# Performance work log

Measured on AMD Instinct MI355X. Metric: run time of the kernel, lower is better.

Reference implementation:

```python
import jax, jax.numpy as jnp
import numpy as np

B, S, D, H = 2, 2048, 1024, 16
HD = D // H  # head dim 64

def setup_inputs() -> dict:
    key = jax.random.key(0)
    k1, k2, k3 = jax.random.split(key, 3)
    x = jax.random.normal(k1, (B, S, D), dtype=jnp.float32)
    w_attn = jax.random.normal(k2, (D, 3 * D), dtype=jnp.float32) * (1.0 / np.sqrt(D))
    w_proj = jax.random.normal(k3, (D, D), dtype=jnp.float32) * (1.0 / np.sqrt(D))
    return {"x": x, "w_attn": w_attn, "w_proj": w_proj}

def reference(x, w_attn, w_proj):
    b, s, d = x.shape
    qkv = x @ w_attn                      # [b, s, 3d]
    q, k, v = jnp.split(qkv, 3, axis=-1)
    def heads(t):
        return t.reshape(b, s, H, HD).transpose(0, 2, 1, 3)  # [b, h, s, hd]
    q, k, v = heads(q), heads(k), heads(v)
    scale = 1.0 / np.sqrt(HD)
    att = jnp.einsum('bhqd,bhkd->bhqk', q, k) * scale        # [b, h, s, s]
    causal = jnp.tril(jnp.ones((s, s), dtype=bool))
    att = jnp.where(causal[None, None], att, -jnp.inf)
    att = jax.nn.softmax(att, axis=-1)
    y = jnp.einsum('bhqk,bhkd->bhqd', att, v)                # [b, h, s, hd]
    y = y.transpose(0, 2, 1, 3).reshape(b, s, d)
    return y @ w_proj
```

## Files before the change

kernel.cpp:

```cpp
#include <hip/hip_runtime.h>

#define B_  2
#define S_  2048
#define D_  1024
#define H_  16
#define HD_ 64
#define TD_ 3072

typedef __bf16 bf16x8 __attribute__((ext_vector_type(8)));
typedef float  f32x4  __attribute__((ext_vector_type(4)));
typedef float  f32x16 __attribute__((ext_vector_type(16)));

#define AS1 __attribute__((address_space(1)))
#define AS3 __attribute__((address_space(3)))

#define MASKVAL (-60000.0f)
#define MINITVAL (-30000.0f)

__device__ __forceinline__ unsigned short f2bf(float f) {
  return __builtin_bit_cast(unsigned short, (__bf16)f);
}

__device__ __forceinline__ unsigned int pkbf(float lo, float hi) {
  unsigned int r;
  asm("v_cvt_pk_bf16_f32 %0, %1, %2" : "=v"(r) : "v"(lo), "v"(hi));
  return r;
}

__device__ __forceinline__ void plswap(unsigned int& a, unsigned int& b) {
  asm volatile("v_permlane32_swap_b32 %0, %1" : "+v"(a), "+v"(b));
}

__device__ __forceinline__ float exp2a(float x) {
  return __builtin_amdgcn_exp2f(x);
}

__device__ __forceinline__ float xmax32(float x) {
  return fmaxf(x, __shfl_xor(x, 32, 64));
}
__device__ __forceinline__ float xadd32(float x) {
  return x + __shfl_xor(x, 32, 64);
}

__device__ __forceinline__ void gload16(const void* g, void* l) {
  __builtin_amdgcn_global_load_lds((const AS1 void*)g, (AS3 void*)l, 16, 0, 0);
}

__global__ __launch_bounds__(256) void k_convert_x(const float* __restrict__ x,
                                                   unsigned short* __restrict__ xb) {
  const int i = (blockIdx.x * 256 + threadIdx.x) * 4;
  float4 v = *(const float4*)(x + i);
  ushort4 o;
  o.x = f2bf(v.x); o.y = f2bf(v.y); o.z = f2bf(v.z); o.w = f2bf(v.w);
  *(ushort4*)(xb + i) = o;
}

__global__ __launch_bounds__(256) void k_prep_w(const float* __restrict__ wa,
                                                const float* __restrict__ wp,
                                                unsigned short* __restrict__ waT,
                                                unsigned short* __restrict__ wpT) {
  __shared__ __align__(16) unsigned short tile[64][72];
  const int t = threadIdx.x;
  const int bx = blockIdx.x;
  const float* w;
  unsigned short* wt;
  int C, c0;
  if (bx < 48) { w = wa; wt = waT; C = TD_; c0 = bx * 64; }
  else         { w = wp; wt = wpT; C = D_;  c0 = (bx - 48) * 64; }
  const int R = D_;
  const int r0 = blockIdx.y * 64;
  const int rr = t >> 2, cc = (t & 3) * 16;
  const float* src = w + (size_t)(r0 + rr) * C + c0 + cc;
#pragma unroll
  for (int j = 0; j < 16; j += 4) {
    float4 v = *(const float4*)(src + j);
    tile[rr][cc + j + 0] = f2bf(v.x);
    tile[rr][cc + j + 1] = f2bf(v.y);
    tile[rr][cc + j + 2] = f2bf(v.z);
    tile[rr][cc + j + 3] = f2bf(v.w);
  }
  __syncthreads();
  unsigned short* dst = wt + (size_t)(c0 + rr) * R + r0 + cc;
#pragma unroll
  for (int j = 0; j < 16; j += 2) {
    unsigned int pk = (unsigned int)tile[cc + j][rr] |
                      ((unsigned int)tile[cc + j + 1][rr] << 16);
    *(unsigned int*)(dst + j) = pk;
  }
}

__global__ __launch_bounds__(256) void k_gemm_qkv(const unsigned short* __restrict__ A,
                                                  const unsigned short* __restrict__ Bt,
                                                  unsigned short* __restrict__ qb,
                                                  unsigned short* __restrict__ kp,
                                                  unsigned short* __restrict__ vp) {
  __shared__ __align__(16) unsigned short ldsA[128 * 64];
  __shared__ __align__(16) unsigned short ldsB[128 * 64];
  const int K = D_;
  const int t = threadIdx.x;
  const int lane = t & 63;
  const int wid = t >> 6;
  const int wr = wid >> 1, wc = wid & 1;
  const int bx = blockIdx.x;
  const int bm = blockIdx.y * 128;
  const int bn = (((bx & 7) * 3) + (bx >> 3)) * 128;
  const int r = lane & 15, g = lane >> 4;

  f32x4 acc[4][4] = {};

  for (int kt = 0; kt < K; kt += 64) {
#pragma unroll
    for (int c = 0; c < 4; ++c) {
      const int idx = c * 256 + t;
      const int row = idx >> 3;
      const int col = ((idx & 7) ^ (row & 7)) * 8;
      gload16(A + (size_t)(bm + row) * K + kt + col, ldsA + idx * 8);
      gload16(Bt + (size_t)(bn + row) * K + kt + col, ldsB + idx * 8);
    }
    asm volatile("s_waitcnt vmcnt(0)" ::: "memory");
    __syncthreads();
#pragma unroll
    for (int ks = 0; ks < 2; ++ks) {
      bf16x8 af[4], bfr[4];
#pragma unroll
      for (int m = 0; m < 4; ++m) {
        const int row = wr * 64 + m * 16 + r;
        const int slot = (ks * 4 + g) ^ (row & 7);
        af[m] = *(const bf16x8*)(ldsA + row * 64 + slot * 8);
      }
#pragma unroll
      for (int n = 0; n < 4; ++n) {
        const int row = wc * 64 + n * 16 + r;
        const int slot = (ks * 4 + g) ^ (row & 7);
        bfr[n] = *(const bf16x8*)(ldsB + row * 64 + slot * 8);
      }
#pragma unroll
      for (int m = 0; m < 4; ++m)
#pragma unroll
        for (int n = 0; n < 4; ++n)
          acc[m][n] = __builtin_amdgcn_mfma_f32_16x16x32_bf16(af[m], bfr[n],
                                                              acc[m][n], 0, 0, 0);
    }
    __syncthreads();
  }

  const int row0 = bm + wr * 64 + g * 4;
  const int col0 = bn + wc * 64 + r;
  const int region = bn >> 10;
  const int b = blockIdx.y >> 4;
  const int sbase = (bm & 2047) + wr * 64 + g * 4;

  if (region == 0) {
#pragma unroll
    for (int m = 0; m < 4; ++m)
#pragma unroll
      for (int n = 0; n < 4; ++n)
#pragma unroll
        for (int i = 0; i < 4; ++i)
          qb[(size_t)(row0 + m * 16 + i) * D_ + col0 + n * 16] = f2bf(acc[m][n][i]);
  } else if (region == 1) {
    const int h = ((bn - 1024) >> 6) + wc;
    unsigned short* kpb = kp + (size_t)(b * 16 + h) * 131072;
#pragma unroll
    for (int m = 0; m < 4; ++m) {
      const int s = sbase + m * 16;
      const int tau = s >> 5, l = s & 31;
#pragma unroll
      for (int n = 0; n < 4; ++n) {
        unsigned short* kq = kpb + tau * 2048 +
                             (n * 64 + (r >> 3) * 32 + l) * 8 + (r & 7);
        kq[0]  = f2bf(acc[m][n][0]);
        kq[8]  = f2bf(acc[m][n][1]);
        kq[16] = f2bf(acc[m][n][2]);
        kq[24] = f2bf(acc[m][n][3]);
      }
    }
  } else {
    const int h = ((bn - 2048) >> 6) + wc;
    unsigned short* vpb = vp + (size_t)(b * 16 + h) * 131072;
#pragma unroll
    for (int m = 0; m < 4; ++m) {
      const int s = sbase + m * 16;
      const int tau2 = s >> 6;
      const int T = (s >> 5) & 1, c16 = (s >> 4) & 1, hi8 = (s >> 3) & 1;
      const int u = s & 7;
#pragma unroll
      for (int n = 0; n < 4; ++n) {
        const int half = n >> 1;
        const int l = (n & 1) * 16 + r;
        const int tid = T * 256 + c16 * 128 + half * 64 + hi8 * 32 + l;
        unsigned long long pk2 =
            (unsigned long long)pkbf(acc[m][n][0], acc[m][n][1]) |
            ((unsigned long long)pkbf(acc[m][n][2], acc[m][n][3]) << 32);
        *(unsigned long long*)(vpb + tau2 * 4096 + tid * 8 + u) = pk2;
      }
    }
  }
}

__global__ __launch_bounds__(256) void k_gemm_bt64(const unsigned short* __restrict__ A,
                                                   const unsigned short* __restrict__ Bt,
                                                   float* __restrict__ C,
                                                   int Ndim, int K) {
  __shared__ __align__(16) unsigned short ldsA[64 * 64];
  __shared__ __align__(16) unsigned short ldsB[128 * 64];
  const int t = threadIdx.x;
  const int lane = t & 63;
  const int wid = t >> 6;
  const int wr = wid >> 1, wc = wid & 1;
  const int bm = blockIdx.y * 64, bn = blockIdx.x * 128;
  const int r = lane & 15, g = lane >> 4;

  f32x4 acc[2][4] = {};

  for (int kt = 0; kt < K; kt += 64) {
#pragma unroll
    for (int c = 0; c < 2; ++c) {
      const int idx = c * 256 + t;
      const int row = idx >> 3;
      const int col = ((idx & 7) ^ (row & 7)) * 8;
      gload16(A + (size_t)(bm + row) * K + kt + col, ldsA + idx * 8);
    }
#pragma unroll
    for (int c = 0; c < 4; ++c) {
      const int idx = c * 256 + t;
      const int row = idx >> 3;
      const int col = ((idx & 7) ^ (row & 7)) * 8;
      gload16(Bt + (size_t)(bn + row) * K + kt + col, ldsB + idx * 8);
    }
    asm volatile("s_waitcnt vmcnt(0)" ::: "memory");
    __syncthreads();
#pragma unroll
    for (int ks = 0; ks < 2; ++ks) {
      bf16x8 af[2], bfr[4];
#pragma unroll
      for (int m = 0; m < 2; ++m) {
        const int row = wr * 32 + m * 16 + r;
        const int slot = (ks * 4 + g) ^ (row & 7);
        af[m] = *(const bf16x8*)(ldsA + row * 64 + slot * 8);
      }
#pragma unroll
      for (int n = 0; n < 4; ++n) {
        const int row = wc * 64 + n * 16 + r;
        const int slot = (ks * 4 + g) ^ (row & 7);
        bfr[n] = *(const bf16x8*)(ldsB + row * 64 + slot * 8);
      }
#pragma unroll
      for (int m = 0; m < 2; ++m)
#pragma unroll
        for (int n = 0; n < 4; ++n)
          acc[m][n] = __builtin_amdgcn_mfma_f32_16x16x32_bf16(af[m], bfr[n],
                                                              acc[m][n], 0, 0, 0);
    }
    __syncthreads();
  }

  const int row0 = bm + wr * 32 + g * 4;
  const int col0 = bn + wc * 64 + r;
#pragma unroll
  for (int m = 0; m < 2; ++m)
#pragma unroll
    for (int n = 0; n < 4; ++n)
#pragma unroll
      for (int i = 0; i < 4; ++i)
        C[(size_t)(row0 + m * 16 + i) * Ndim + col0 + n * 16] = acc[m][n][i];
}

__global__ __launch_bounds__(256, 4) void k_attn(const unsigned short* __restrict__ qb,
                                                 const unsigned short* __restrict__ kp,
                                                 const unsigned short* __restrict__ vp,
                                                 unsigned short* __restrict__ y) {
  __shared__ __align__(16) float Om[2][64][32];
  __shared__ float Ml[2][2][32];
  const int t = threadIdx.x;
  const int lane = t & 63, w = t >> 6;
  const int l31 = lane & 31, hi = lane >> 5;
  const int pr = w & 1;
  const int parity = w >> 1;
  const int bh = blockIdx.x & 31;
  const int j = blockIdx.x >> 5;
  const int sj = pr ? (63 - j) : j;
  const int h = bh & 15, b = bh >> 4;
  const int qbase = 32 * sj;
  const int qq = qbase + l31;

  const float SC = 0.125f * 1.44269504f;

  bf16x8 qf[4];
  {
    const unsigned short* qp = qb + (size_t)(b * S_ + qbase + l31) * D_ + h * HD_;
#pragma unroll
    for (int c = 0; c < 4; ++c) {
      bf16x8 rl = *(const bf16x8*)(qp + c * 16 + hi * 8);
      union { unsigned int u[4]; bf16x8 v; } pl;
#pragma unroll
      for (int jx = 0; jx < 4; ++jx)
        pl.u[jx] = pkbf((float)rl[2 * jx] * SC, (float)rl[2 * jx + 1] * SC);
      qf[c] = pl.v;
    }
  }

  float mr = MINITVAL, lr = 0.f;
  f32x16 o0 = {}, o1 = {};

  const unsigned short* kpb = kp + (size_t)bh * 131072;
  const unsigned short* vpb = vp + (size_t)bh * 131072;

  const int tmax = (32 * sj + 31) >> 6;

  for (int kvt = parity; kvt <= tmax; kvt += 2) {
    const int kv0 = kvt << 6;
    bf16x8 kf[2][4];
#pragma unroll
    for (int T = 0; T < 2; ++T)
#pragma unroll
      for (int c = 0; c < 4; ++c)
        kf[T][c] = *(const bf16x8*)(kpb + (size_t)(kvt * 8 + T * 4 + c) * 512 +
                                    lane * 8);

    f32x16 s0 = {}, s1 = {};
    __builtin_amdgcn_s_setprio(1);
#pragma unroll
    for (int c = 0; c < 4; ++c) {
      s0 = __builtin_amdgcn_mfma_f32_32x32x16_bf16(kf[0][c], qf[c], s0, 0, 0, 0);
      s1 = __builtin_amdgcn_mfma_f32_32x32x16_bf16(kf[1][c], qf[c], s1, 0, 0, 0);
    }
    __builtin_amdgcn_s_setprio(0);

    float am[4] = {MASKVAL, MASKVAL, MASKVAL, MASKVAL};
    if (kv0 + 63 > qbase) {
#pragma unroll
      for (int rg = 0; rg < 16; ++rg) {
        const int kv = kv0 + (rg & 3) + 8 * (rg >> 2) + 4 * hi;
        float v0 = (kv <= qq) ? s0[rg] : MASKVAL; s0[rg] = v0;
        float v1 = (kv + 32 <= qq) ? s1[rg] : MASKVAL; s1[rg] = v1;
        am[rg & 3] = fmaxf(am[rg & 3], fmaxf(v0, v1));
      }
    } else {
#pragma unroll
      for (int rg = 0; rg < 16; ++rg)
        am[rg & 3] = fmaxf(am[rg & 3], fmaxf(s0[rg], s1[rg]));
    }
    const float pm = xmax32(fmaxf(fmaxf(am[0], am[1]), fmaxf(am[2], am[3])));

    const float nm = fmaxf(mr, pm);
    if (!__all(nm - mr <= 12.0f)) {
      const float cr = exp2a(mr - nm);
      mr = nm;
      lr *= cr;
#pragma unroll
      for (int rg = 0; rg < 16; ++rg) { o0[rg] *= cr; o1[rg] *= cr; }
    }

    float as[4] = {0.f, 0.f, 0.f, 0.f};
#pragma unroll
    for (int rg = 0; rg < 16; ++rg) {
      const float p0 = exp2a(s0[rg] - mr); s0[rg] = p0;
      const float p1 = exp2a(s1[rg] - mr); s1[rg] = p1;
      as[rg & 3] += p0 + p1;
    }
    lr += xadd32((as[0] + as[1]) + (as[2] + as[3]));

    const unsigned short* vpt = vpb + (size_t)kvt * 4096;
    __builtin_amdgcn_s_setprio(1);
#pragma unroll
    for (int T = 0; T < 2; ++T) {
      const f32x16& sT = T ? s1 : s0;
#pragma unroll
      for (int c = 0; c < 2; ++c) {
        unsigned int x0 = pkbf(sT[8 * c + 0], sT[8 * c + 1]);
        unsigned int x1 = pkbf(sT[8 * c + 2], sT[8 * c + 3]);
        unsigned int x2 = pkbf(sT[8 * c + 4], sT[8 * c + 5]);
        unsigned int x3 = pkbf(sT[8 * c + 6], sT[8 * c + 7]);
        plswap(x0, x2);
        plswap(x1, x3);
        union { unsigned int u[4]; bf16x8 v; } pb;
        pb.u[0] = x0; pb.u[1] = x1; pb.u[2] = x2; pb.u[3] = x3;
        const unsigned short* vb = vpt + (size_t)((T * 2 + c) * 2) * 512 + lane * 8;
        bf16x8 vf0 = *(const bf16x8*)(vb);
        bf16x8 vf1 = *(const bf16x8*)(vb + 512);
        o0 = __builtin_amdgcn_mfma_f32_32x32x16_bf16(vf0, pb.v, o0, 0, 0, 0);
        o1 = __builtin_amdgcn_mfma_f32_32x32x16_bf16(vf1, pb.v, o1, 0, 0, 0);
      }
    }
    __builtin_amdgcn_s_setprio(0);
  }

  __syncthreads();
  if (parity) {
#pragma unroll
    for (int tt = 0; tt < 2; ++tt) {
      const f32x16& o = tt ? o1 : o0;
#pragma unroll
      for (int rg = 0; rg < 16; ++rg) {
        const int row = tt * 32 + (rg & 3) + 8 * (rg >> 2) + 4 * hi;
        Om[pr][row][l31] = o[rg];
      }
    }
    if (!hi) {
      Ml[pr][0][l31] = mr;
      Ml[pr][1][l31] = lr;
    }
  }
  __syncthreads();
  if (!parity) {
    const float mo = Ml[pr][0][l31];
    const float lo2 = Ml[pr][1][l31];
    const float mm = fmaxf(mr, mo);
    const float ce = exp2a(mr - mm), co = exp2a(mo - mm);
    const float lt = lr * ce + lo2 * co;
    const float ic = ce / lt, io = co / lt;
    unsigned short* yp = y + (size_t)(b * S_ + qbase + l31) * D_ + h * HD_;
#pragma unroll
    for (int tt = 0; tt < 2; ++tt) {
      const f32x16& o = tt ? o1 : o0;
#pragma unroll
      for (int rg = 0; rg < 16; rg += 2) {
        const int row = tt * 32 + (rg & 3) + 8 * (rg >> 2) + 4 * hi;
        const float v0 = o[rg] * ic + Om[pr][row][l31] * io;
        const float v1 = o[rg + 1] * ic + Om[pr][row + 1][l31] * io;
        *(unsigned int*)(yp + row) = pkbf(v0, v1);
      }
    }
  }
}

extern "C" void kernel_launch(void* const* d_in, const int* in_sizes, int n_in,
                              void* d_out, int out_size, void* d_ws, size_t ws_size,
                              hipStream_t stream) {
  const float* x  = (const float*)d_in[0];
  const float* wa = (const float*)d_in[1];
  const float* wp = (const float*)d_in[2];
  float* out = (float*)d_out;

  char* ws = (char*)d_ws;
  unsigned short* xb  = (unsigned short*)(ws + 0);
  unsigned short* waT = (unsigned short*)(ws + 8388608);
  unsigned short* wpT = (unsigned short*)(ws + 14680064);
  unsigned short* qb  = (unsigned short*)(ws + 16777216);
  unsigned short* kp  = (unsigned short*)(ws + 25165824);
  unsigned short* vp  = (unsigned short*)(ws + 33554432);
  unsigned short* yb  = (unsigned short*)(ws + 41943040);

  k_convert_x<<<4096, 256, 0, stream>>>(x, xb);
  k_prep_w<<<dim3(64, 16), 256, 0, stream>>>(wa, wp, waT, wpT);
  k_gemm_qkv<<<dim3(24, 32), 256, 0, stream>>>(xb, waT, qb, kp, vp);
  k_attn<<<1024, 256, 0, stream>>>(qb, kp, vp, yb);
  k_gemm_bt64<<<dim3(8, 64), 256, 0, stream>>>(yb, wpT, out, D_, D_);
}
```

Measured before the change: 115.3 us.

## Pre-pack QKV GEMM operands into MFMA fragment layout and drop LDS staging

The x conversion and w_attn transpose kernels now write bf16 operands directly in a 16x32 MFMA fragment-tiled layout. The QKV GEMM then loads each lane's 8-element fragment straight from global memory with one 16-byte load, removing LDS staging, swizzling and barriers. This trades LDS reuse across waves for direct global/L2 reads, so each wave re-fetches operands that were previously shared within the block, and there is no software prefetch of upcoming k-chunks.

Result: slower. 119.6 us (+3.8%).

```diff
diff --git a/kernel.cpp b/kernel.cpp
--- a/kernel.cpp
+++ b/kernel.cpp
@@ -47,27 +47,35 @@
 }
 
 __global__ __launch_bounds__(256) void k_convert_x(const float* __restrict__ x,
-                                                   unsigned short* __restrict__ xb) {
-  const int i = (blockIdx.x * 256 + threadIdx.x) * 4;
-  float4 v = *(const float4*)(x + i);
-  ushort4 o;
-  o.x = f2bf(v.x); o.y = f2bf(v.y); o.z = f2bf(v.z); o.w = f2bf(v.w);
-  *(ushort4*)(xb + i) = o;
+                                                   unsigned short* __restrict__ ap) {
+  const int t = threadIdx.x;
+  const int bid = blockIdx.x;
+  const int mt = bid >> 3, kcg = bid & 7;
+  const int rr = t >> 4, q = t & 15;
+  const int row = mt * 16 + rr;
+  const int c0 = kcg * 128 + q * 8;
+  const float4 v0 = *(const float4*)(x + (size_t)row * D_ + c0);
+  const float4 v1 = *(const float4*)(x + (size_t)row * D_ + c0 + 4);
+  const int kc = c0 >> 5, g = (c0 >> 3) & 3;
+  uint4 o;
+  o.x = pkbf(v0.x, v0.y);
+  o.y = pkbf(v0.z, v0.w);
+  o.z = pkbf(v1.x, v1.y);
+  o.w = pkbf(v1.z, v1.w);
+  *(uint4*)(ap + ((size_t)mt * 32 + kc) * 512 + (g * 16 + rr) * 8) = o;
 }
 
 __global__ __launch_bounds__(256) void k_prep_w(const float* __restrict__ wa,
                                                 const float* __restrict__ wp,
-                                                unsigned short* __restrict__ waT,
+                                                unsigned short* __restrict__ bp,
                                                 unsigned short* __restrict__ wpT) {
   __shared__ __align__(16) unsigned short tile[64][72];
   const int t = threadIdx.x;
   const int bx = blockIdx.x;
-  const float* w;
-  unsigned short* wt;
-  int C, c0;
-  if (bx < 48) { w = wa; wt = waT; C = TD_; c0 = bx * 64; }
-  else         { w = wp; wt = wpT; C = D_;  c0 = (bx - 48) * 64; }
-  const int R = D_;
+  const bool isA = (bx < 48);
+  const float* w = isA ? wa : wp;
+  const int C = isA ? TD_ : D_;
+  const int c0 = (isA ? bx : bx - 48) * 64;
   const int r0 = blockIdx.y * 64;
   const int rr = t >> 2, cc = (t & 3) * 16;
   const float* src = w + (size_t)(r0 + rr) * C + c0 + cc;
@@ -80,23 +88,36 @@
     tile[rr][cc + j + 3] = f2bf(v.w);
   }
   __syncthreads();
-  unsigned short* dst = wt + (size_t)(c0 + rr) * R + r0 + cc;
-#pragma unroll
-  for (int j = 0; j < 16; j += 2) {
-    unsigned int pk = (unsigned int)tile[cc + j][rr] |
-                      ((unsigned int)tile[cc + j + 1][rr] << 16);
-    *(unsigned int*)(dst + j) = pk;
-  }
-}
-
-__global__ __launch_bounds__(256) void k_gemm_qkv(const unsigned short* __restrict__ A,
-                                                  const unsigned short* __restrict__ Bt,
+  if (isA) {
+    const int nt = (c0 + rr) >> 4, n15 = rr & 15;
+#pragma unroll
+    for (int gg = 0; gg < 2; ++gg) {
+      const int kk = cc + gg * 8;
+      const int kglob = r0 + kk;
+      const int kc = kglob >> 5, g = (kglob >> 3) & 3;
+      uint4 o;
+      o.x = (unsigned int)tile[kk + 0][rr] | ((unsigned int)tile[kk + 1][rr] << 16);
+      o.y = (unsigned int)tile[kk + 2][rr] | ((unsigned int)tile[kk + 3][rr] << 16);
+      o.z = (unsigned int)tile[kk + 4][rr] | ((unsigned int)tile[kk + 5][rr] << 16);
+      o.w = (unsigned int)tile[kk + 6][rr] | ((unsigned int)tile[kk + 7][rr] << 16);
+      *(uint4*)(bp + ((size_t)nt * 32 + kc) * 512 + (g * 16 + n15) * 8) = o;
+    }
+  } else {
+    unsigned short* dst = wpT + (size_t)(c0 + rr) * D_ + r0 + cc;
+#pragma unroll
+    for (int j = 0; j < 16; j += 2) {
+      unsigned int pk = (unsigned int)tile[cc + j][rr] |
+                        ((unsigned int)tile[cc + j + 1][rr] << 16);
+      *(unsigned int*)(dst + j) = pk;
+    }
+  }
+}
+
+__global__ __launch_bounds__(256) void k_gemm_qkv(const unsigned short* __restrict__ Ap,
+                                                  const unsigned short* __restrict__ Bp,
                                                   unsigned short* __restrict__ qb,
                                                   unsigned short* __restrict__ kp,
                                                   unsigned short* __restrict__ vp) {
-  __shared__ __align__(16) unsigned short ldsA[128 * 64];
-  __shared__ __align__(16) unsigned short ldsB[128 * 64];
-  const int K = D_;
   const int t = threadIdx.x;
   const int lane = t & 63;
   const int wid = t >> 6;
@@ -105,43 +126,25 @@
   const int bm = blockIdx.y * 128;
   const int bn = (((bx & 7) * 3) + (bx >> 3)) * 128;
   const int r = lane & 15, g = lane >> 4;
+  const int mt0 = (bm + wr * 64) >> 4;
+  const int nt0 = (bn + wc * 64) >> 4;
 
   f32x4 acc[4][4] = {};
 
-  for (int kt = 0; kt < K; kt += 64) {
-#pragma unroll
-    for (int c = 0; c < 4; ++c) {
-      const int idx = c * 256 + t;
-      const int row = idx >> 3;
-      const int col = ((idx & 7) ^ (row & 7)) * 8;
-      gload16(A + (size_t)(bm + row) * K + kt + col, ldsA + idx * 8);
-      gload16(Bt + (size_t)(bn + row) * K + kt + col, ldsB + idx * 8);
-    }
-    asm volatile("s_waitcnt vmcnt(0)" ::: "memory");
-    __syncthreads();
-#pragma unroll
-    for (int ks = 0; ks < 2; ++ks) {
-      bf16x8 af[4], bfr[4];
-#pragma unroll
-      for (int m = 0; m < 4; ++m) {
-        const int row = wr * 64 + m * 16 + r;
-        const int slot = (ks * 4 + g) ^ (row & 7);
-        af[m] = *(const bf16x8*)(ldsA + row * 64 + slot * 8);
-      }
-#pragma unroll
-      for (int n = 0; n < 4; ++n) {
-        const int row = wc * 64 + n * 16 + r;
-        const int slot = (ks * 4 + g) ^ (row & 7);
-        bfr[n] = *(const bf16x8*)(ldsB + row * 64 + slot * 8);
-      }
-#pragma unroll
-      for (int m = 0; m < 4; ++m)
-#pragma unroll
-        for (int n = 0; n < 4; ++n)
-          acc[m][n] = __builtin_amdgcn_mfma_f32_16x16x32_bf16(af[m], bfr[n],
-                                                              acc[m][n], 0, 0, 0);
-    }
-    __syncthreads();
+  for (int kc = 0; kc < 32; ++kc) {
+    bf16x8 af[4], bfr[4];
+#pragma unroll
+    for (int m = 0; m < 4; ++m)
+      af[m] = *(const bf16x8*)(Ap + ((size_t)(mt0 + m) * 32 + kc) * 512 + lane * 8);
+#pragma unroll
+    for (int n = 0; n < 4; ++n)
+      bfr[n] = *(const bf16x8*)(Bp + ((size_t)(nt0 + n) * 32 + kc) * 512 + lane * 8);
+#pragma unroll
+    for (int m = 0; m < 4; ++m)
+#pragma unroll
+      for (int n = 0; n < 4; ++n)
+        acc[m][n] = __builtin_amdgcn_mfma_f32_16x16x32_bf16(af[m], bfr[n],
+                                                            acc[m][n], 0, 0, 0);
   }
 
   const int row0 = bm + wr * 64 + g * 4;
@@ -434,17 +437,17 @@
   float* out = (float*)d_out;
 
   char* ws = (char*)d_ws;
-  unsigned short* xb  = (unsigned short*)(ws + 0);
-  unsigned short* waT = (unsigned short*)(ws + 8388608);
+  unsigned short* ap  = (unsigned short*)(ws + 0);
+  unsigned short* bp  = (unsigned short*)(ws + 8388608);
   unsigned short* wpT = (unsigned short*)(ws + 14680064);
   unsigned short* qb  = (unsigned short*)(ws + 16777216);
   unsigned short* kp  = (unsigned short*)(ws + 25165824);
   unsigned short* vp  = (unsigned short*)(ws + 33554432);
   unsigned short* yb  = (unsigned short*)(ws + 41943040);
 
-  k_convert_x<<<4096, 256, 0, stream>>>(x, xb);
-  k_prep_w<<<dim3(64, 16), 256, 0, stream>>>(wa, wp, waT, wpT);
-  k_gemm_qkv<<<dim3(24, 32), 256, 0, stream>>>(xb, waT, qb, kp, vp);
+  k_convert_x<<<2048, 256, 0, stream>>>(x, ap);
+  k_prep_w<<<dim3(64, 16), 256, 0, stream>>>(wa, wp, bp, wpT);
+  k_gemm_qkv<<<dim3(24, 32), 256, 0, stream>>>(ap, bp, qb, kp, vp);
   k_attn<<<1024, 256, 0, stream>>>(qb, kp, vp, yb);
   k_gemm_bt64<<<dim3(8, 64), 256, 0, stream>>>(yb, wpT, out, D_, D_);
 }
```
